# Optimization experiments

Hardware: AMD Instinct MI355X
Metric: run time of the kernel (lower is better)

The kernel has to match this reference:

```python
import jax, jax.numpy as jnp
import numpy as np

N_HEAD = 16
HEAD_SIZE = 64  # n_embd // n_head = 1024 // 16


def setup_inputs() -> dict:
    key = jax.random.key(0)
    k1, k2 = jax.random.split(key)
    B, T, C = 2, 2048, 1024
    x = jax.random.normal(k1, (B, T, C), dtype=jnp.float32)
    w_attn = jax.random.normal(k2, (C, 3 * C), dtype=jnp.float32) * (C ** -0.5)
    b_attn = jnp.zeros((3 * C,), dtype=jnp.float32)
    return {"x": x, "w_attn": w_attn, "b_attn": b_attn}


def reference(x, w_attn, b_attn):
    B, T, C = x.shape
    qkv = x @ w_attn + b_attn  # [B, T, 3C]
    q, k, v = jnp.split(qkv, 3, axis=-1)
    # [B, T, H, D] -> [B, H, T, D]
    def heads(t):
        return t.reshape(B, T, N_HEAD, HEAD_SIZE).transpose(0, 2, 1, 3)
    q, k, v = heads(q), heads(k), heads(v)
    scale = HEAD_SIZE ** -0.5
    wei = jnp.einsum('bhqd,bhkd->bhqk', q, k) * scale  # [B, H, T, T]
    causal = jnp.tril(jnp.ones((T, T), dtype=bool))
    wei = jnp.where(causal, wei, -jnp.inf)
    wei = jax.nn.softmax(wei, axis=-1)
    out = jnp.einsum('bhqk,bhkd->bhqd', wei, v)  # [B, H, T, D]
    out = out.transpose(0, 2, 1, 3).reshape(B, T, C)
    return out
```

## Files before the change

### kernel.cpp

```cpp
#include <hip/hip_runtime.h>
#include <hip/hip_bf16.h>

#define BSZ 2
#define SEQ 2048
#define CDIM 1024
#define NHEAD 16
#define HDIM 64
#define M_GEMM (BSZ * SEQ)
#define N_GEMM (3 * CDIM)
#define K_GEMM CDIM
#define QK_PITCH (2 * CDIM)

typedef __attribute__((ext_vector_type(8))) short short8;
typedef __attribute__((ext_vector_type(4))) short short4v;
typedef __attribute__((ext_vector_type(4))) float f32x4;

__device__ __forceinline__ short bf16_rn(float f) {
    unsigned u = __builtin_bit_cast(unsigned, f);
    u += 0x7FFF + ((u >> 16) & 1);
    return (short)(u >> 16);
}

__device__ __forceinline__ void gl2lds16(const short* g, short* l) {
    __builtin_amdgcn_global_load_lds(
        (const __attribute__((address_space(1))) unsigned int*)g,
        (__attribute__((address_space(3))) unsigned int*)l, 16, 0, 0);
}

#define WAITV4() asm volatile("s_waitcnt vmcnt(4)")
#define WAITV0() asm volatile("s_waitcnt vmcnt(0)")
#define LGKM0()  asm volatile("s_waitcnt lgkmcnt(0)")
#define SCB()    __builtin_amdgcn_sched_barrier(0)
#define BARRIER() __builtin_amdgcn_s_barrier()

__global__ __launch_bounds__(256) void cvt_fused(const float* __restrict__ X,
                                                 const float* __restrict__ W,
                                                 short* __restrict__ Xb,
                                                 short* __restrict__ WT) {
    const int tid = threadIdx.x;
    if (blockIdx.x < 2048) {
        size_t idx = ((size_t)blockIdx.x * 256 + tid) * 8;
        float4 a = *(const float4*)&X[idx];
        float4 b = *(const float4*)&X[idx + 4];
        short8 o;
        o[0] = bf16_rn(a.x); o[1] = bf16_rn(a.y); o[2] = bf16_rn(a.z); o[3] = bf16_rn(a.w);
        o[4] = bf16_rn(b.x); o[5] = bf16_rn(b.y); o[6] = bf16_rn(b.z); o[7] = bf16_rn(b.w);
        *(short8*)&Xb[idx] = o;
        return;
    }
    __shared__ short T[64][72];
    const int bid = blockIdx.x - 2048;
    const int n0 = (bid % 48) * 64;
    const int k0 = (bid / 48) * 64;
#pragma unroll
    for (int pass = 0; pass < 4; ++pass) {
        int i = pass * 256 + tid;
        int kr = i >> 4;
        int n4 = i & 15;
        float4 v = *(const float4*)&W[(size_t)(k0 + kr) * N_GEMM + n0 + n4 * 4];
        T[n4 * 4 + 0][kr] = bf16_rn(v.x);
        T[n4 * 4 + 1][kr] = bf16_rn(v.y);
        T[n4 * 4 + 2][kr] = bf16_rn(v.z);
        T[n4 * 4 + 3][kr] = bf16_rn(v.w);
    }
    __syncthreads();
#pragma unroll
    for (int pass = 0; pass < 2; ++pass) {
        int o = pass * 256 + tid;
        int nr = o >> 3;
        int c8 = o & 7;
        *(short8*)&WT[(size_t)(n0 + nr) * K_GEMM + k0 + c8 * 8] =
            *(const short8*)&T[nr][c8 * 8];
    }
}

#define MFMA_QUAD(MB, NB)                                                     \
    do {                                                                      \
        __builtin_amdgcn_s_setprio(1);                                        \
        _Pragma("unroll")                                                     \
        for (int mi_ = 0; mi_ < 4; ++mi_)                                     \
            _Pragma("unroll")                                                 \
            for (int ni_ = 0; ni_ < 2; ++ni_)                                 \
                _Pragma("unroll")                                             \
                for (int ks_ = 0; ks_ < 2; ++ks_)                             \
                    acc[(MB) + mi_][(NB) + ni_] =                             \
                        __builtin_amdgcn_mfma_f32_16x16x32_bf16(              \
                            Af[mi_][ks_], Bf[(NB) + ni_][ks_],                \
                            acc[(MB) + mi_][(NB) + ni_], 0, 0, 0);            \
        __builtin_amdgcn_s_setprio(0);                                        \
    } while (0)

__global__ __launch_bounds__(512, 2) void qkv_gemm_8ph(const short* __restrict__ A,
                                                       const short* __restrict__ Bt,
                                                       const float* __restrict__ bias,
                                                       short* __restrict__ Yqk,
                                                       short* __restrict__ Yv) {
    __shared__ short Asl[32768];
    __shared__ short Bsl[32768];

    const int tid  = threadIdx.x;
    const int w    = tid >> 6;
    const int lane = tid & 63;
    const int l16  = lane & 15;
    const int quad = lane >> 4;
    const int wm   = w >> 2;
    const int wn   = w & 3;
    const int ls   = lane >> 3;
    const int lc   = lane & 7;
    const int fsw  = l16 & 7;

    const int orig = blockIdx.y * 12 + blockIdx.x;
    const int xcd  = orig & 7;
    const int idx  = orig >> 3;
    const int bM   = ((xcd & 1) << 3) + (idx & 7);
    const int bN   = (xcd >> 1) * 3 + (idx >> 3);
    const int m0   = bM << 8;
    const int n0   = bN << 8;

    const short* Ab = A  + (size_t)m0 * K_GEMM;
    const short* Bb = Bt + (size_t)n0 * K_GEMM;

    f32x4 acc[8][4];
#pragma unroll
    for (int i = 0; i < 8; ++i)
#pragma unroll
        for (int j = 0; j < 4; ++j) acc[i][j] = (f32x4){0.f, 0.f, 0.f, 0.f};

    auto stageA = [&](int unit, int tt, int sbuf) {
#pragma unroll
        for (int i = 0; i < 2; ++i) {
            const int u0 = (i * 8 + w) * 8;
            const int tr = (u0 & 63) + ((u0 >> 6) << 7) + unit * 64;
            gl2lds16(Ab + (size_t)(tr + ls) * K_GEMM + tt * 64 + ((lc ^ ls) << 3),
                     &Asl[sbuf * 16384 + tr * 64]);
        }
    };
    auto stageB = [&](int unit, int tt, int sbuf) {
#pragma unroll
        for (int i = 0; i < 2; ++i) {
            const int u0 = (i * 8 + w) * 8;
            const int tr = (u0 & 31) + ((u0 >> 5) << 6) + unit * 32;
            gl2lds16(Bb + (size_t)(tr + ls) * K_GEMM + tt * 64 + ((lc ^ ls) << 3),
                     &Bsl[sbuf * 16384 + tr * 64]);
        }
    };
    auto rdA = [&](int ab, int mi, int ks) -> short8 {
        const int r = wm * 128 + mi * 16 + l16;
        return *(const short8*)&Asl[ab + r * 64 + ((ks * 4 + quad) ^ fsw) * 8];
    };
    auto rdB = [&](int ab, int ni, int ks) -> short8 {
        const int r = wn * 64 + ni * 16 + l16;
        return *(const short8*)&Bsl[ab + r * 64 + ((ks * 4 + quad) ^ fsw) * 8];
    };

    stageA(0, 0, 0);
    stageB(0, 0, 0);
    stageB(1, 0, 0);
    stageA(1, 0, 0);
    WAITV4();
    SCB();
    BARRIER();
    SCB();

    for (int t = 0; t < 16; ++t) {
        const int buf = t & 1;
        const int sb  = buf ^ 1;
        const int tn  = (t + 1) & 15;
        const int ab  = buf * 16384;

        short8 Af[4][2], Bf[4][2];

#pragma unroll
        for (int mi = 0; mi < 4; ++mi)
#pragma unroll
            for (int ks = 0; ks < 2; ++ks) Af[mi][ks] = rdA(ab, mi, ks);
#pragma unroll
        for (int ni = 0; ni < 2; ++ni)
#pragma unroll
            for (int ks = 0; ks < 2; ++ks) Bf[ni][ks] = rdB(ab, ni, ks);
        stageA(0, tn, sb);
        SCB(); BARRIER(); LGKM0(); SCB();
        MFMA_QUAD(0, 0);
        WAITV4();
        SCB(); BARRIER(); SCB();

#pragma unroll
        for (int ni = 2; ni < 4; ++ni)
#pragma unroll
            for (int ks = 0; ks < 2; ++ks) Bf[ni][ks] = rdB(ab, ni, ks);
        stageB(0, tn, sb);
        SCB(); BARRIER(); LGKM0(); SCB();
        MFMA_QUAD(0, 2);
        WAITV4();
        SCB(); BARRIER(); SCB();

#pragma unroll
        for (int mi = 0; mi < 4; ++mi)
#pragma unroll
            for (int ks = 0; ks < 2; ++ks) Af[mi][ks] = rdA(ab, 4 + mi, ks);
        stageB(1, tn, sb);
        SCB(); BARRIER(); LGKM0(); SCB();
        MFMA_QUAD(4, 0);
        SCB(); BARRIER(); SCB();

        stageA(1, tn, sb);
        SCB(); BARRIER(); SCB();
        MFMA_QUAD(4, 2);
        WAITV4();
        SCB(); BARRIER(); SCB();
    }
    WAITV0();

    if (n0 >= 2 * CDIM) {
#pragma unroll
        for (int mi = 0; mi < 8; ++mi) {
            int row0 = m0 + wm * 128 + mi * 16 + quad * 4;
#pragma unroll
            for (int ni = 0; ni < 4; ++ni) {
                int colg = n0 + wn * 64 + ni * 16 + l16;
                float bb = bias[colg];
                short4v pk;
#pragma unroll
                for (int r = 0; r < 4; ++r) pk[r] = bf16_rn(acc[mi][ni][r] + bb);
                *(short4v*)&Yv[(size_t)(colg - 2 * CDIM) * M_GEMM + row0] = pk;
            }
        }
    } else {
        const float qs = (n0 < CDIM) ? 0.125f * 1.44269504f : 1.0f;
#pragma unroll
        for (int mi = 0; mi < 8; ++mi)
#pragma unroll
            for (int r = 0; r < 4; ++r) {
                int row = m0 + wm * 128 + mi * 16 + quad * 4 + r;
#pragma unroll
                for (int ni = 0; ni < 4; ++ni) {
                    int colg = n0 + wn * 64 + ni * 16 + l16;
                    Yqk[(size_t)row * QK_PITCH + colg] =
                        bf16_rn((acc[mi][ni][r] + bias[colg]) * qs);
                }
            }
    }
}

__global__ __launch_bounds__(256) void attn_mfma(const short* __restrict__ qk,
                                                 const short* __restrict__ vT,
                                                 float* __restrict__ out) {
    const int b = blockIdx.z;
    const int h = blockIdx.y;
    const int bx = blockIdx.x;
    const int u = h + 16 * b;
    const int band = u >> 3;
    const int base = (band & 2) ? ((bx + 16) & 31) : bx;
    const int qt = (band & 1) ? (31 - base) : base;
    const int tid = threadIdx.x;
    const int w = tid >> 6;
    const int lane = tid & 63;
    const int quad = lane >> 4;
    const int l16 = lane & 15;
    const int q0 = qt * 64;

    __shared__ short Ks[2][64 * 64];
    __shared__ short Vt[2][64 * 64];

    int koff[2], voff[2], ldso[2];
#pragma unroll
    for (int p = 0; p < 2; ++p) {
        int cid = p * 256 + w * 64 + lane;
        int row = cid >> 3;
        int hK = (row & 3) | (((row >> 3) & 1) << 2);
        int cK = (cid & 7) ^ hK;
        int cV = (cid & 7) ^ (row & 7);
        koff[p] = row * QK_PITCH + cK * 8;
        voff[p] = row * M_GEMM + cV * 8;
        ldso[p] = (p * 256 + w * 64) * 8;
    }

    const short* qrow = qk + (size_t)(b * SEQ + q0 + w * 16 + l16) * QK_PITCH + h * HDIM;
    short8 aq[2];
    aq[0] = *(const short8*)(qrow + quad * 8);
    aq[1] = *(const short8*)(qrow + 32 + quad * 8);

    float l_run = 0.f;
    f32x4 o_acc[4];
#pragma unroll
    for (int dt = 0; dt < 4; ++dt) o_acc[dt] = (f32x4){0.f, 0.f, 0.f, 0.f};

    const int qglob = q0 + w * 16 + l16;
    const short* kb0 = qk + (size_t)(b * SEQ) * QK_PITCH + CDIM + h * HDIM;
    const short* vb0 = vT + (size_t)(h * HDIM) * M_GEMM + b * SEQ;

    const int ksl = l16 & 7;

    const int Fq = ((l16 >> 2) << 3) + (l16 & 3);

#pragma unroll
    for (int p = 0; p < 2; ++p) {
        gl2lds16(kb0 + koff[p], &Ks[0][ldso[p]]);
        gl2lds16(vb0 + voff[p], &Vt[0][ldso[p]]);
    }
    __syncthreads();

    for (int kt = 0; kt <= qt; ++kt) {
        const int cur = kt & 1;

        if (kt < qt) {
            const short* kbase = kb0 + (size_t)(kt + 1) * 64 * QK_PITCH;
            const short* vbase = vb0 + (kt + 1) * 64;
#pragma unroll
            for (int p = 0; p < 2; ++p) {
                gl2lds16(kbase + koff[p], &Ks[cur ^ 1][ldso[p]]);
                gl2lds16(vbase + voff[p], &Vt[cur ^ 1][ldso[p]]);
            }
        }

        const short* KsC = Ks[cur];
        const short* VtC = Vt[cur];

        f32x4 s[4];
#pragma unroll
        for (int nt = 0; nt < 4; ++nt) s[nt] = (f32x4){0.f, 0.f, 0.f, 0.f};
        __builtin_amdgcn_s_setprio(1);
#pragma unroll
        for (int nt = 0; nt < 4; ++nt) {
            const int F  = (nt >> 1) * 32 + (nt & 1) * 4 + Fq;
            const int hF = (F & 3) | (((F >> 3) & 1) << 2);
#pragma unroll
            for (int ks = 0; ks < 2; ++ks) {
                short8 kf = *(const short8*)&KsC[F * 64 + (((ks * 4 + quad) ^ hF) * 8)];
                s[nt] = __builtin_amdgcn_mfma_f32_16x16x32_bf16(kf, aq[ks], s[nt], 0, 0, 0);
            }
        }
        __builtin_amdgcn_s_setprio(0);

        short8 pa0, pa1;
        float lsum = 0.f;
        if (kt < qt) {
#pragma unroll
            for (int nt = 0; nt < 4; ++nt)
#pragma unroll
                for (int r = 0; r < 4; ++r) {
                    float pp = __builtin_amdgcn_exp2f(s[nt][r]);
                    lsum += pp;
                    short pb = bf16_rn(pp);
                    if (nt < 2) pa0[(nt & 1) * 4 + r] = pb;
                    else        pa1[(nt & 1) * 4 + r] = pb;
                }
        } else {
#pragma unroll
            for (int nt = 0; nt < 4; ++nt)
#pragma unroll
                for (int r = 0; r < 4; ++r) {
                    int key = kt * 64 + (nt >> 1) * 32 + quad * 8 + (nt & 1) * 4 + r;
                    float pp = __builtin_amdgcn_exp2f(s[nt][r]);
                    pp = (key > qglob) ? 0.f : pp;
                    lsum += pp;
                    short pb = bf16_rn(pp);
                    if (nt < 2) pa0[(nt & 1) * 4 + r] = pb;
                    else        pa1[(nt & 1) * 4 + r] = pb;
                }
        }
        l_run += lsum;

        __builtin_amdgcn_s_setprio(1);
#pragma unroll
        for (int dt = 0; dt < 4; ++dt)
#pragma unroll
            for (int ks = 0; ks < 2; ++ks) {
                short8 bv = *(const short8*)&VtC[(dt * 16 + l16) * 64 +
                                                 ((ks * 4 + quad) ^ ksl) * 8];
                o_acc[dt] = __builtin_amdgcn_mfma_f32_16x16x32_bf16(
                    ks ? pa1 : pa0, bv, o_acc[dt], 0, 0, 0);
            }
        __builtin_amdgcn_s_setprio(0);

        __syncthreads();
    }

    float l = l_run;
    l += __shfl_xor(l, 16);
    l += __shfl_xor(l, 32);
#pragma unroll
    for (int r = 0; r < 4; ++r) {
        float lq = __shfl(l, quad * 4 + r);
        float inv = 1.f / lq;
        int row = q0 + w * 16 + quad * 4 + r;
        float* optr = out + (size_t)(b * SEQ + row) * CDIM + h * HDIM;
#pragma unroll
        for (int dt = 0; dt < 4; ++dt)
            optr[dt * 16 + l16] = o_acc[dt][r] * inv;
    }
}

extern "C" void kernel_launch(void* const* d_in, const int* in_sizes, int n_in,
                              void* d_out, int out_size, void* d_ws, size_t ws_size,
                              hipStream_t stream) {
    const float* x      = (const float*)d_in[0];
    const float* w_attn = (const float*)d_in[1];
    const float* b_attn = (const float*)d_in[2];
    float* out = (float*)d_out;

    short* qk  = (short*)d_ws;
    short* vT  = (short*)((char*)d_ws + 16777216);
    short* xb  = (short*)((char*)d_ws + 25165824);
    short* wT  = (short*)((char*)d_ws + 33554432);

    cvt_fused<<<2048 + 768, 256, 0, stream>>>(x, w_attn, xb, wT);

    dim3 g1(N_GEMM / 256, M_GEMM / 256);
    qkv_gemm_8ph<<<g1, 512, 0, stream>>>(xb, wT, b_attn, qk, vT);

    dim3 g2(SEQ / 64, NHEAD, BSZ);
    attn_mfma<<<g2, 256, 0, stream>>>(qk, vT, out);
}
```

Baseline: 153.6 us.

## Shrink QKV GEMM N-tile to 192 to fill all CUs

The QKV projection GEMM drops from 256x256 tiles to 256x192 tiles. The grid grows from 12x16 to 16x16 blocks so more workgroups are available to spread across the GPU's compute units. B staging is split into even and odd chunks with new LDS row mapping, the vmcnt waits are rebalanced, and the epilogue now picks the Q/K/V destination per column since a tile can straddle a Q/K/V boundary. The trade-off is less reuse of each loaded A tile and a per-column branch in the epilogue.

```diff
diff --git a/kernel.cpp b/kernel.cpp
--- a/kernel.cpp
+++ b/kernel.cpp
@@ -27,7 +27,8 @@
         (__attribute__((address_space(3))) unsigned int*)l, 16, 0, 0);
 }
 
-#define WAITV4() asm volatile("s_waitcnt vmcnt(4)")
+#define WAITV2() asm volatile("s_waitcnt vmcnt(2)")
+#define WAITV3() asm volatile("s_waitcnt vmcnt(3)")
 #define WAITV0() asm volatile("s_waitcnt vmcnt(0)")
 #define LGKM0()  asm volatile("s_waitcnt lgkmcnt(0)")
 #define SCB()    __builtin_amdgcn_sched_barrier(0)
@@ -74,29 +75,13 @@
     }
 }
 
-#define MFMA_QUAD(MB, NB)                                                     \
-    do {                                                                      \
-        __builtin_amdgcn_s_setprio(1);                                        \
-        _Pragma("unroll")                                                     \
-        for (int mi_ = 0; mi_ < 4; ++mi_)                                     \
-            _Pragma("unroll")                                                 \
-            for (int ni_ = 0; ni_ < 2; ++ni_)                                 \
-                _Pragma("unroll")                                             \
-                for (int ks_ = 0; ks_ < 2; ++ks_)                             \
-                    acc[(MB) + mi_][(NB) + ni_] =                             \
-                        __builtin_amdgcn_mfma_f32_16x16x32_bf16(              \
-                            Af[mi_][ks_], Bf[(NB) + ni_][ks_],                \
-                            acc[(MB) + mi_][(NB) + ni_], 0, 0, 0);            \
-        __builtin_amdgcn_s_setprio(0);                                        \
-    } while (0)
-
 __global__ __launch_bounds__(512, 2) void qkv_gemm_8ph(const short* __restrict__ A,
                                                        const short* __restrict__ Bt,
                                                        const float* __restrict__ bias,
                                                        short* __restrict__ Yqk,
                                                        short* __restrict__ Yv) {
     __shared__ short Asl[32768];
-    __shared__ short Bsl[32768];
+    __shared__ short Bsl[24576];
 
     const int tid  = threadIdx.x;
     const int w    = tid >> 6;
@@ -109,22 +94,22 @@
     const int lc   = lane & 7;
     const int fsw  = l16 & 7;
 
-    const int orig = blockIdx.y * 12 + blockIdx.x;
+    const int orig = blockIdx.y * 16 + blockIdx.x;
     const int xcd  = orig & 7;
     const int idx  = orig >> 3;
     const int bM   = ((xcd & 1) << 3) + (idx & 7);
-    const int bN   = (xcd >> 1) * 3 + (idx >> 3);
+    const int bN   = (xcd >> 1) * 4 + (idx >> 3);
     const int m0   = bM << 8;
-    const int n0   = bN << 8;
+    const int n0   = bN * 192;
 
     const short* Ab = A  + (size_t)m0 * K_GEMM;
     const short* Bb = Bt + (size_t)n0 * K_GEMM;
 
-    f32x4 acc[8][4];
+    f32x4 acc[8][3];
 #pragma unroll
     for (int i = 0; i < 8; ++i)
 #pragma unroll
-        for (int j = 0; j < 4; ++j) acc[i][j] = (f32x4){0.f, 0.f, 0.f, 0.f};
+        for (int j = 0; j < 3; ++j) acc[i][j] = (f32x4){0.f, 0.f, 0.f, 0.f};
 
     auto stageA = [&](int unit, int tt, int sbuf) {
 #pragma unroll
@@ -135,40 +120,47 @@
                      &Asl[sbuf * 16384 + tr * 64]);
         }
     };
-    auto stageB = [&](int unit, int tt, int sbuf) {
+    auto stageBE = [&](int tt, int sbuf) {
 #pragma unroll
         for (int i = 0; i < 2; ++i) {
-            const int u0 = (i * 8 + w) * 8;
-            const int tr = (u0 & 31) + ((u0 >> 5) << 6) + unit * 32;
-            gl2lds16(Bb + (size_t)(tr + ls) * K_GEMM + tt * 64 + ((lc ^ ls) << 3),
-                     &Bsl[sbuf * 16384 + tr * 64]);
-        }
+            const int jb = i * 64 + w * 8;
+            const int gr = (jb >> 5) * 48 + (jb & 31);
+            gl2lds16(Bb + (size_t)(gr + ls) * K_GEMM + tt * 64 + ((lc ^ ls) << 3),
+                     &Bsl[sbuf * 12288 + jb * 64]);
+        }
+    };
+    auto stageBO = [&](int tt, int sbuf) {
+        const int t8 = w * 8;
+        const int jb = 128 + t8;
+        const int gr = (t8 >> 4) * 48 + 32 + (t8 & 15);
+        gl2lds16(Bb + (size_t)(gr + ls) * K_GEMM + tt * 64 + ((lc ^ ls) << 3),
+                 &Bsl[sbuf * 12288 + jb * 64]);
     };
     auto rdA = [&](int ab, int mi, int ks) -> short8 {
         const int r = wm * 128 + mi * 16 + l16;
         return *(const short8*)&Asl[ab + r * 64 + ((ks * 4 + quad) ^ fsw) * 8];
     };
-    auto rdB = [&](int ab, int ni, int ks) -> short8 {
-        const int r = wn * 64 + ni * 16 + l16;
-        return *(const short8*)&Bsl[ab + r * 64 + ((ks * 4 + quad) ^ fsw) * 8];
+    auto rdB = [&](int bb, int ni, int ks) -> short8 {
+        const int j = (ni < 2) ? (wn * 32 + ni * 16 + l16)
+                               : (128 + wn * 16 + l16);
+        return *(const short8*)&Bsl[bb + j * 64 + ((ks * 4 + quad) ^ fsw) * 8];
     };
 
     stageA(0, 0, 0);
-    stageB(0, 0, 0);
-    stageB(1, 0, 0);
+    stageBE(0, 0);
     stageA(1, 0, 0);
-    WAITV4();
-    SCB();
-    BARRIER();
-    SCB();
+    stageBO(0, 0);
+    WAITV3();
+    SCB(); BARRIER(); SCB();
 
     for (int t = 0; t < 16; ++t) {
         const int buf = t & 1;
         const int sb  = buf ^ 1;
         const int tn  = (t + 1) & 15;
         const int ab  = buf * 16384;
-
-        short8 Af[4][2], Bf[4][2];
+        const int bb  = buf * 12288;
+
+        short8 Af[4][2], Bf[3][2];
 
 #pragma unroll
         for (int mi = 0; mi < 4; ++mi)
@@ -177,68 +169,92 @@
 #pragma unroll
         for (int ni = 0; ni < 2; ++ni)
 #pragma unroll
-            for (int ks = 0; ks < 2; ++ks) Bf[ni][ks] = rdB(ab, ni, ks);
+            for (int ks = 0; ks < 2; ++ks) Bf[ni][ks] = rdB(bb, ni, ks);
         stageA(0, tn, sb);
         SCB(); BARRIER(); LGKM0(); SCB();
-        MFMA_QUAD(0, 0);
-        WAITV4();
+        __builtin_amdgcn_s_setprio(1);
+#pragma unroll
+        for (int mi = 0; mi < 4; ++mi)
+#pragma unroll
+            for (int ni = 0; ni < 2; ++ni)
+#pragma unroll
+                for (int ks = 0; ks < 2; ++ks)
+                    acc[mi][ni] = __builtin_amdgcn_mfma_f32_16x16x32_bf16(
+                        Af[mi][ks], Bf[ni][ks], acc[mi][ni], 0, 0, 0);
+        __builtin_amdgcn_s_setprio(0);
+        WAITV2();
         SCB(); BARRIER(); SCB();
 
 #pragma unroll
-        for (int ni = 2; ni < 4; ++ni)
-#pragma unroll
-            for (int ks = 0; ks < 2; ++ks) Bf[ni][ks] = rdB(ab, ni, ks);
-        stageB(0, tn, sb);
+        for (int ks = 0; ks < 2; ++ks) Bf[2][ks] = rdB(bb, 2, ks);
+        stageBE(tn, sb);
         SCB(); BARRIER(); LGKM0(); SCB();
-        MFMA_QUAD(0, 2);
-        WAITV4();
+        __builtin_amdgcn_s_setprio(1);
+#pragma unroll
+        for (int mi = 0; mi < 4; ++mi)
+#pragma unroll
+            for (int ks = 0; ks < 2; ++ks)
+                acc[mi][2] = __builtin_amdgcn_mfma_f32_16x16x32_bf16(
+                    Af[mi][ks], Bf[2][ks], acc[mi][2], 0, 0, 0);
+        __builtin_amdgcn_s_setprio(0);
         SCB(); BARRIER(); SCB();
 
 #pragma unroll
         for (int mi = 0; mi < 4; ++mi)
 #pragma unroll
             for (int ks = 0; ks < 2; ++ks) Af[mi][ks] = rdA(ab, 4 + mi, ks);
-        stageB(1, tn, sb);
+        stageA(1, tn, sb);
         SCB(); BARRIER(); LGKM0(); SCB();
-        MFMA_QUAD(4, 0);
+        __builtin_amdgcn_s_setprio(1);
+#pragma unroll
+        for (int mi = 0; mi < 4; ++mi)
+#pragma unroll
+            for (int ni = 0; ni < 2; ++ni)
+#pragma unroll
+                for (int ks = 0; ks < 2; ++ks)
+                    acc[4 + mi][ni] = __builtin_amdgcn_mfma_f32_16x16x32_bf16(
+                        Af[mi][ks], Bf[ni][ks], acc[4 + mi][ni], 0, 0, 0);
+        __builtin_amdgcn_s_setprio(0);
         SCB(); BARRIER(); SCB();
 
-        stageA(1, tn, sb);
+        stageBO(tn, sb);
         SCB(); BARRIER(); SCB();
-        MFMA_QUAD(4, 2);
-        WAITV4();
+        __builtin_amdgcn_s_setprio(1);
+#pragma unroll
+        for (int mi = 0; mi < 4; ++mi)
+#pragma unroll
+            for (int ks = 0; ks < 2; ++ks)
+                acc[4 + mi][2] = __builtin_amdgcn_mfma_f32_16x16x32_bf16(
+                    Af[mi][ks], Bf[2][ks], acc[4 + mi][2], 0, 0, 0);
+        __builtin_amdgcn_s_setprio(0);
+        WAITV3();
         SCB(); BARRIER(); SCB();
     }
     WAITV0();
 
-    if (n0 >= 2 * CDIM) {
-#pragma unroll
-        for (int mi = 0; mi < 8; ++mi) {
-            int row0 = m0 + wm * 128 + mi * 16 + quad * 4;
-#pragma unroll
-            for (int ni = 0; ni < 4; ++ni) {
-                int colg = n0 + wn * 64 + ni * 16 + l16;
-                float bb = bias[colg];
+    const float log2e8 = 0.125f * 1.44269504f;
+#pragma unroll
+    for (int mi = 0; mi < 8; ++mi) {
+#pragma unroll
+        for (int ni = 0; ni < 3; ++ni) {
+            const int colg = n0 + wn * 48 + ni * 16 + l16;
+            const float bb2 = bias[colg];
+            if (colg >= 2 * CDIM) {
+                const int row0 = m0 + wm * 128 + mi * 16 + quad * 4;
                 short4v pk;
 #pragma unroll
-                for (int r = 0; r < 4; ++r) pk[r] = bf16_rn(acc[mi][ni][r] + bb);
+                for (int r = 0; r < 4; ++r) pk[r] = bf16_rn(acc[mi][ni][r] + bb2);
                 *(short4v*)&Yv[(size_t)(colg - 2 * CDIM) * M_GEMM + row0] = pk;
-            }
-        }
-    } else {
-        const float qs = (n0 < CDIM) ? 0.125f * 1.44269504f : 1.0f;
-#pragma unroll
-        for (int mi = 0; mi < 8; ++mi)
-#pragma unroll
-            for (int r = 0; r < 4; ++r) {
-                int row = m0 + wm * 128 + mi * 16 + quad * 4 + r;
-#pragma unroll
-                for (int ni = 0; ni < 4; ++ni) {
-                    int colg = n0 + wn * 64 + ni * 16 + l16;
+            } else {
+                const float qs = (colg < CDIM) ? log2e8 : 1.0f;
+#pragma unroll
+                for (int r = 0; r < 4; ++r) {
+                    const int row = m0 + wm * 128 + mi * 16 + quad * 4 + r;
                     Yqk[(size_t)row * QK_PITCH + colg] =
-                        bf16_rn((acc[mi][ni][r] + bias[colg]) * qs);
+                        bf16_rn((acc[mi][ni][r] + bb2) * qs);
                 }
             }
+        }
     }
 }
 
@@ -406,7 +422,7 @@
 
     cvt_fused<<<2048 + 768, 256, 0, stream>>>(x, w_attn, xb, wT);
 
-    dim3 g1(N_GEMM / 256, M_GEMM / 256);
+    dim3 g1(N_GEMM / 192, M_GEMM / 256);
     qkv_gemm_8ph<<<g1, 512, 0, stream>>>(xb, wT, b_attn, qk, vT);
 
     dim3 g2(SEQ / 64, NHEAD, BSZ);
```

New measurement: 152.5 us. About the same (-0.7%).
